# Kernel optimization log

Measured on AMD Instinct MI355X. Metric: run time of the kernel, lower is better.

Reference implementation:

```python
import jax, jax.numpy as jnp
import numpy as np

EPS = 1e-12


def qsplit(x):
    # [..., 4n] with block layout [r|i|j|k] -> [..., n, 4]
    s = x.shape
    n = s[-1] // 4
    return jnp.swapaxes(x.reshape(s[:-1] + (4, n)), -1, -2)


def qmerge(q):
    # [..., n, 4] -> [..., 4n] block layout (transpose(-1,-2).view in torch)
    s = q.shape
    return jnp.swapaxes(q, -1, -2).reshape(s[:-2] + (s[-2] * 4,))


def qnormalize(q):
    # F.normalize(p=2, dim=-1)
    n = jnp.linalg.norm(q, axis=-1, keepdims=True)
    return q / jnp.maximum(n, EPS)


def qmul(q, r):
    # Hamilton product, last axis = (w, x, y, z)
    qw, qx, qy, qz = q[..., 0], q[..., 1], q[..., 2], q[..., 3]
    rw, rx, ry, rz = r[..., 0], r[..., 1], r[..., 2], r[..., 3]
    return jnp.stack([
        qw * rw - qx * rx - qy * ry - qz * rz,
        qw * rx + qx * rw + qy * rz - qz * ry,
        qw * ry - qx * rz + qy * rw + qz * rx,
        qw * rz + qx * ry - qy * rx + qz * rw,
    ], axis=-1)


def qlinear(x, W, b=None):
    # quaternion linear: x [..., 4*n_in], W [4, n_in, n_out]
    xr, xi, xj, xk = jnp.split(x, 4, axis=-1)
    Wr, Wi, Wj, Wk = W[0], W[1], W[2], W[3]
    out = jnp.concatenate([
        xr @ Wr - xi @ Wi - xj @ Wj - xk @ Wk,
        xr @ Wi + xi @ Wr + xj @ Wk - xk @ Wj,
        xr @ Wj - xi @ Wk + xj @ Wr + xk @ Wi,
        xr @ Wk + xi @ Wj - xj @ Wi + xk @ Wr,
    ], axis=-1)
    return out if b is None else out + b


def setup_inputs() -> dict:
    key = jax.random.key(0)
    ks = jax.random.split(key, 7)
    T_enc, T_tgt, B, D, H = 100, 26, 512, 96, 1024
    d4, h4 = D // 4, H // 4
    inp = jax.random.normal(ks[0], (T_enc, B, D), dtype=jnp.float32)
    target = jax.random.normal(ks[1], (T_tgt, B, D), dtype=jnp.float32)
    Wx = jax.random.normal(ks[2], (4, d4, h4), dtype=jnp.float32) * 0.05
    bx = jnp.zeros((H,), dtype=jnp.float32)
    Wh = jax.random.normal(ks[3], (4, h4, h4), dtype=jnp.float32) * 0.05
    Wl = jax.random.normal(ks[4], (4, h4, d4), dtype=jnp.float32) * 0.05
    bl = jnp.zeros((D,), dtype=jnp.float32)
    return {"inp": inp, "target": target, "Wx": Wx, "bx": bx, "Wh": Wh, "Wl": Wl, "bl": bl}


def reference(inp, target, Wx, bx, Wh, Wl, bl):
    B = inp.shape[1]
    H = Wh.shape[1] * 4

    def rnn_step(h, xt):
        h_new = jnp.tanh(qlinear(xt, Wx, bx) + qlinear(h, Wh))
        return h_new, h_new

    def predict(hseq, pre):
        # quaternion linear + per-quaternion L2 normalize + residual Hamilton product
        pred = qlinear(hseq, Wl, bl)
        qn = qnormalize(qsplit(pred))
        return qmerge(qmul(qn, qsplit(pre)))

    h0 = jnp.zeros((B, H), dtype=inp.dtype)
    h_last, hs = jax.lax.scan(rnn_step, h0, inp)  # hs: [T_enc, B, H]
    out_enc = predict(hs, inp)

    def dec_step(carry, _):
        h, x = carry
        h_new = jnp.tanh(qlinear(x, Wx, bx) + qlinear(h, Wh))
        pred = predict(h_new, x)
        return (h_new, pred), pred

    T_dec = target.shape[0] - 1
    _, out_dec = jax.lax.scan(dec_step, (h_last, target[0]), None, length=T_dec)
    return out_enc, out_dec
```

## Files before the change

kernel.cpp:

```cpp
#include <hip/hip_runtime.h>
#include <hip/hip_bf16.h>
#include <cstdint>

#define TENC 100
#define TDEC 25
#define BATCH 512
#define DIN 96
#define HDIM 1024

__device__ __constant__ int q_widx[4][4] = {{0,1,2,3},{1,0,3,2},{2,3,0,1},{3,2,1,0}};
__device__ __constant__ float q_sgn[4][4] = {{1.f,-1.f,-1.f,-1.f},
                                             {1.f, 1.f, 1.f,-1.f},
                                             {1.f,-1.f, 1.f, 1.f},
                                             {1.f, 1.f,-1.f, 1.f}};

__global__ void build_eff_kernel(const float* __restrict__ W, float* __restrict__ M,
                                 int nin, int nout) {
    int idx = blockIdx.x * blockDim.x + threadIdx.x;
    int ncol = nout * 4;
    int total = nin * 4 * ncol;
    if (idx >= total) return;
    int col = idx % ncol;
    int k = idx / ncol;
    int c = k / nin, m = k - c * nin;
    int comp = col / nout, o = col - comp * nout;
    M[idx] = q_sgn[comp][c] * W[(size_t)(q_widx[comp][c] * nin + m) * nout + o];
}

__device__ inline float xla_tanh(float x) {
    float ax = fabsf(x);
    if (ax < 0.0004f) return x;
    float t = fminf(fmaxf(x, -7.99881172180175781f), 7.99881172180175781f);
    float x2 = __fmul_rn(t, t);
    float p = -2.76076847742355e-16f;
    p = __fadd_rn(__fmul_rn(p, x2), 2.00018790482477e-13f);
    p = __fadd_rn(__fmul_rn(p, x2), -8.60467152213735e-11f);
    p = __fadd_rn(__fmul_rn(p, x2), 5.12229709037114e-08f);
    p = __fadd_rn(__fmul_rn(p, x2), 1.48572235717979e-05f);
    p = __fadd_rn(__fmul_rn(p, x2), 6.37261928875436e-04f);
    p = __fadd_rn(__fmul_rn(p, x2), 4.89352455891786e-03f);
    float num = __fmul_rn(t, p);
    float q = 1.19825839466702e-06f;
    q = __fadd_rn(__fmul_rn(q, x2), 1.18534705686654e-04f);
    q = __fadd_rn(__fmul_rn(q, x2), 2.26843463243900e-03f);
    q = __fadd_rn(__fmul_rn(q, x2), 4.89352518554385e-03f);
    return __fdiv_rn(num, q);
}

__global__ __launch_bounds__(256)
void rnn_part(const float* __restrict__ X,
              const float* __restrict__ Hin,
              const float* __restrict__ Mx,
              const float* __restrict__ Mh,
              float* __restrict__ part) {
    __shared__ __align__(16) float As[64][68];
    __shared__ __align__(16) float Bs[64][64];

    const int tid = threadIdx.x;
    const int tx = tid & 15, ty = tid >> 4;
    const int c0 = blockIdx.x * 64;
    const int r0 = blockIdx.y * 64;
    const int z  = blockIdx.z;
    const int lk = tid & 63, lr = tid >> 6;

    float acc[4][4];
    #pragma unroll
    for (int i = 0; i < 4; ++i)
        #pragma unroll
        for (int j = 0; j < 4; ++j) acc[i][j] = 0.f;

    if (z < 4) {
        for (int kb = 0; kb < 4; ++kb) {
            const int k0 = z * 256 + kb * 64;
            __syncthreads();
            {
                const float* ap = Hin + (size_t)(r0 + lr) * 1024 + k0 + lk;
                #pragma unroll
                for (int i = 0; i < 16; ++i)
                    As[lk][lr + 4 * i] = ap[(size_t)(4 * i) * 1024];
            }
            {
                const int ccol = c0 + lk;
                #pragma unroll
                for (int i = 0; i < 16; ++i) {
                    int k = lr + 4 * i;
                    Bs[k][lk] = Mh[(size_t)(k0 + k) * 1024 + ccol];
                }
            }
            __syncthreads();
            #pragma unroll 8
            for (int k = 0; k < 64; ++k) {
                float4 av = *reinterpret_cast<const float4*>(&As[k][ty * 4]);
                float4 bv = *reinterpret_cast<const float4*>(&Bs[k][tx * 4]);
                float aa[4] = {av.x, av.y, av.z, av.w};
                float bb[4] = {bv.x, bv.y, bv.z, bv.w};
                #pragma unroll
                for (int i = 0; i < 4; ++i)
                    #pragma unroll
                    for (int j = 0; j < 4; ++j)
                        acc[i][j] = __fadd_rn(acc[i][j], __fmul_rn(aa[i], bb[j]));
            }
        }
    } else {
        for (int c = 0; c < 4; ++c) {
            float xa[4][4];
            #pragma unroll
            for (int i = 0; i < 4; ++i)
                #pragma unroll
                for (int j = 0; j < 4; ++j) xa[i][j] = 0.f;
            const int k0 = c * 24;
            __syncthreads();
            if (lk < 24) {
                const float* ap = X + (size_t)(r0 + lr) * 96 + k0 + lk;
                #pragma unroll
                for (int i = 0; i < 16; ++i)
                    As[lk][lr + 4 * i] = ap[(size_t)(4 * i) * 96];
            }
            {
                const int ccol = c0 + lk;
                #pragma unroll
                for (int i = 0; i < 16; ++i) {
                    int k = lr + 4 * i;
                    if (k < 24)
                        Bs[k][lk] = Mx[(size_t)(k0 + k) * 1024 + ccol];
                }
            }
            __syncthreads();
            #pragma unroll 4
            for (int k = 0; k < 24; ++k) {
                float4 av = *reinterpret_cast<const float4*>(&As[k][ty * 4]);
                float4 bv = *reinterpret_cast<const float4*>(&Bs[k][tx * 4]);
                float aa[4] = {av.x, av.y, av.z, av.w};
                float bb[4] = {bv.x, bv.y, bv.z, bv.w};
                #pragma unroll
                for (int i = 0; i < 4; ++i)
                    #pragma unroll
                    for (int j = 0; j < 4; ++j)
                        xa[i][j] = __fadd_rn(xa[i][j], __fmul_rn(aa[i], bb[j]));
            }
            #pragma unroll
            for (int i = 0; i < 4; ++i)
                #pragma unroll
                for (int j = 0; j < 4; ++j)
                    acc[i][j] = __fadd_rn(acc[i][j], xa[i][j]);
        }
    }

    float* pp = part + (size_t)z * (BATCH * HDIM);
    const int ccol = c0 + tx * 4;
    #pragma unroll
    for (int i = 0; i < 4; ++i) {
        int r = r0 + ty * 4 + i;
        *reinterpret_cast<float4*>(pp + (size_t)r * 1024 + ccol) =
            make_float4(acc[i][0], acc[i][1], acc[i][2], acc[i][3]);
    }
}

__global__ __launch_bounds__(256)
void rnn_combine(const float* __restrict__ part, const float* __restrict__ bx,
                 float* __restrict__ Hout) {
    int t = blockIdx.x * blockDim.x + threadIdx.x;
    int i = t * 4;
    int col = i & 1023;
    const size_t SH = (size_t)BATCH * HDIM;
    float4 xp = *reinterpret_cast<const float4*>(part + 4 * SH + i);
    float4 h0 = *reinterpret_cast<const float4*>(part + 0 * SH + i);
    float4 h1 = *reinterpret_cast<const float4*>(part + 1 * SH + i);
    float4 h2 = *reinterpret_cast<const float4*>(part + 2 * SH + i);
    float4 h3 = *reinterpret_cast<const float4*>(part + 3 * SH + i);
    float4 bb = *reinterpret_cast<const float4*>(bx + col);
    float o[4];
    {
        float xpv[4] = {xp.x, xp.y, xp.z, xp.w};
        float h0v[4] = {h0.x, h0.y, h0.z, h0.w};
        float h1v[4] = {h1.x, h1.y, h1.z, h1.w};
        float h2v[4] = {h2.x, h2.y, h2.z, h2.w};
        float h3v[4] = {h3.x, h3.y, h3.z, h3.w};
        float bv[4]  = {bb.x, bb.y, bb.z, bb.w};
        #pragma unroll
        for (int j = 0; j < 4; ++j) {
            float hcb = __fadd_rn(__fadd_rn(__fadd_rn(h0v[j], h1v[j]), h2v[j]), h3v[j]);
            float rs  = __fadd_rn(__fadd_rn(xpv[j], bv[j]), hcb);
            o[j] = xla_tanh(rs);
        }
    }
    *reinterpret_cast<float4*>(Hout + i) = make_float4(o[0], o[1], o[2], o[3]);
}

__global__ __launch_bounds__(256)
void predict_part(const float* __restrict__ H,
                  const float* __restrict__ Ml,
                  float* __restrict__ ppart) {
    __shared__ float lds[8576];
    float* As = lds;
    float* Bs = lds + 2176;

    const int tid = threadIdx.x;
    const int tx = tid & 15, ty = tid >> 4;
    const int r0 = blockIdx.x * 32;
    const int z  = blockIdx.y;

    float acc[2][6];
    #pragma unroll
    for (int i = 0; i < 2; ++i)
        #pragma unroll
        for (int j = 0; j < 6; ++j) acc[i][j] = 0.f;

    for (int kb = 0; kb < 4; ++kb) {
        const int k0 = z * 256 + kb * 64;
        __syncthreads();
        {
            int lk = tid & 63, lr0 = tid >> 6;
            #pragma unroll
            for (int i = 0; i < 8; ++i) {
                int row = lr0 + 4 * i;
                As[lk * 34 + row] = H[(size_t)(r0 + row) * 1024 + k0 + lk];
            }
        }
        #pragma unroll
        for (int i = 0; i < 24; ++i) {
            int idx = tid + 256 * i;
            int k = idx / 96, c = idx - k * 96;
            Bs[k * 100 + c] = Ml[(size_t)(k0 + k) * 96 + c];
        }
        __syncthreads();
        #pragma unroll 4
        for (int k = 0; k < 64; ++k) {
            float2 a = *reinterpret_cast<const float2*>(&As[k * 34 + ty * 2]);
            const float* bp = &Bs[k * 100 + tx * 6];
            float2 b0 = *reinterpret_cast<const float2*>(bp);
            float2 b1 = *reinterpret_cast<const float2*>(bp + 2);
            float2 b2 = *reinterpret_cast<const float2*>(bp + 4);
            float bv[6] = {b0.x, b0.y, b1.x, b1.y, b2.x, b2.y};
            #pragma unroll
            for (int j = 0; j < 6; ++j) {
                acc[0][j] = __fadd_rn(acc[0][j], __fmul_rn(a.x, bv[j]));
                acc[1][j] = __fadd_rn(acc[1][j], __fmul_rn(a.y, bv[j]));
            }
        }
    }

    float* pp = ppart + (size_t)z * (BATCH * DIN);
    #pragma unroll
    for (int i = 0; i < 2; ++i)
        #pragma unroll
        for (int j = 0; j < 6; ++j)
            pp[(size_t)(r0 + ty * 2 + i) * 96 + tx * 6 + j] = acc[i][j];
}

__global__ void combine_qmul(const float* __restrict__ ppart,
                             const float* __restrict__ bl,
                             const float* __restrict__ pre,
                             float* __restrict__ out, int M) {
    int q = blockIdx.x * blockDim.x + threadIdx.x;
    if (q >= M * 24) return;
    int b = q / 24, n = q - b * 24;
    const size_t SP = (size_t)BATCH * DIN;
    float pq[4];
    #pragma unroll
    for (int comp = 0; comp < 4; ++comp) {
        size_t idx = (size_t)b * 96 + comp * 24 + n;
        float p0 = ppart[0 * SP + idx];
        float p1 = ppart[1 * SP + idx];
        float p2 = ppart[2 * SP + idx];
        float p3 = ppart[3 * SP + idx];
        pq[comp] = __fadd_rn(__fadd_rn(__fadd_rn(__fadd_rn(p0, p1), p2), p3),
                             bl[comp * 24 + n]);
    }
    float pw = pq[0], px = pq[1], py = pq[2], pz = pq[3];
    float s = __fadd_rn(__fadd_rn(__fadd_rn(__fmul_rn(pw, pw), __fmul_rn(px, px)),
                                  __fmul_rn(py, py)), __fmul_rn(pz, pz));
    float nr = sqrtf(s);
    float nm = fmaxf(nr, 1e-12f);
    pw = __fdiv_rn(pw, nm); px = __fdiv_rn(px, nm);
    py = __fdiv_rn(py, nm); pz = __fdiv_rn(pz, nm);
    const float* r = pre + (size_t)b * 96 + n;
    float rw = r[0], rx = r[24], ry = r[48], rz = r[72];
    float* o = out + (size_t)b * 96 + n;
    o[0]  = __fsub_rn(__fsub_rn(__fsub_rn(__fmul_rn(pw, rw), __fmul_rn(px, rx)),
                                __fmul_rn(py, ry)), __fmul_rn(pz, rz));
    o[24] = __fsub_rn(__fadd_rn(__fadd_rn(__fmul_rn(pw, rx), __fmul_rn(px, rw)),
                                __fmul_rn(py, rz)), __fmul_rn(pz, ry));
    o[48] = __fadd_rn(__fadd_rn(__fsub_rn(__fmul_rn(pw, ry), __fmul_rn(px, rz)),
                                __fmul_rn(py, rw)), __fmul_rn(pz, rx));
    o[72] = __fadd_rn(__fsub_rn(__fadd_rn(__fmul_rn(pw, rz), __fmul_rn(px, ry)),
                                __fmul_rn(py, rx)), __fmul_rn(pz, rw));
}

__global__ __launch_bounds__(256)
void predict_qmul(const float* __restrict__ H,
                  const float* __restrict__ Ml,
                  const float* __restrict__ bl,
                  const float* __restrict__ pre,
                  float* __restrict__ out) {
    __shared__ float lds[8576];
    float* As = lds;
    float* Bs = lds + 2176;
    float* Ps = lds;

    const int tid = threadIdx.x;
    const int tx = tid & 15, ty = tid >> 4;
    const int r0 = blockIdx.x * 32;

    float hcb[2][6], ha[2][6];
    #pragma unroll
    for (int i = 0; i < 2; ++i)
        #pragma unroll
        for (int j = 0; j < 6; ++j) { hcb[i][j] = 0.f; ha[i][j] = 0.f; }

    for (int kb = 0; kb < 16; ++kb) {
        __syncthreads();
        {
            int lk = tid & 63, lr0 = tid >> 6;
            #pragma unroll
            for (int i = 0; i < 8; ++i) {
                int row = lr0 + 4 * i;
                As[lk * 34 + row] = H[(size_t)(r0 + row) * 1024 + kb * 64 + lk];
            }
        }
        #pragma unroll
        for (int i = 0; i < 24; ++i) {
            int idx = tid + 256 * i;
            int k = idx / 96, c = idx - k * 96;
            Bs[k * 100 + c] = Ml[(size_t)(kb * 64 + k) * 96 + c];
        }
        __syncthreads();
        #pragma unroll 4
        for (int k = 0; k < 64; ++k) {
            float2 a = *reinterpret_cast<const float2*>(&As[k * 34 + ty * 2]);
            const float* bp = &Bs[k * 100 + tx * 6];
            float2 b0 = *reinterpret_cast<const float2*>(bp);
            float2 b1 = *reinterpret_cast<const float2*>(bp + 2);
            float2 b2 = *reinterpret_cast<const float2*>(bp + 4);
            float bv[6] = {b0.x, b0.y, b1.x, b1.y, b2.x, b2.y};
            #pragma unroll
            for (int j = 0; j < 6; ++j) {
                ha[0][j] = __fadd_rn(ha[0][j], __fmul_rn(a.x, bv[j]));
                ha[1][j] = __fadd_rn(ha[1][j], __fmul_rn(a.y, bv[j]));
            }
        }
        if ((kb & 3) == 3) {
            #pragma unroll
            for (int i = 0; i < 2; ++i)
                #pragma unroll
                for (int j = 0; j < 6; ++j) {
                    hcb[i][j] = __fadd_rn(hcb[i][j], ha[i][j]);
                    ha[i][j] = 0.f;
                }
        }
    }

    __syncthreads();
    #pragma unroll
    for (int i = 0; i < 2; ++i)
        #pragma unroll
        for (int j = 0; j < 6; ++j) {
            int c = tx * 6 + j;
            Ps[(ty * 2 + i) * 100 + c] = __fadd_rn(hcb[i][j], bl[c]);
        }
    __syncthreads();

    #pragma unroll
    for (int i = 0; i < 3; ++i) {
        int q = tid + 256 * i;
        int row = q / 24, n = q - row * 24;
        const float* p = &Ps[row * 100 + n];
        float pw = p[0], px = p[24], py = p[48], pz = p[72];
        float s = __fadd_rn(__fadd_rn(__fadd_rn(__fmul_rn(pw, pw), __fmul_rn(px, px)),
                                      __fmul_rn(py, py)), __fmul_rn(pz, pz));
        float nr = sqrtf(s);
        float nm = fmaxf(nr, 1e-12f);
        pw = __fdiv_rn(pw, nm); px = __fdiv_rn(px, nm);
        py = __fdiv_rn(py, nm); pz = __fdiv_rn(pz, nm);
        const float* r = pre + (size_t)(r0 + row) * 96 + n;
        float rw = r[0], rx = r[24], ry = r[48], rz = r[72];
        float* o = out + (size_t)(r0 + row) * 96 + n;
        o[0]  = __fsub_rn(__fsub_rn(__fsub_rn(__fmul_rn(pw, rw), __fmul_rn(px, rx)),
                                    __fmul_rn(py, ry)), __fmul_rn(pz, rz));
        o[24] = __fsub_rn(__fadd_rn(__fadd_rn(__fmul_rn(pw, rx), __fmul_rn(px, rw)),
                                    __fmul_rn(py, rz)), __fmul_rn(pz, ry));
        o[48] = __fadd_rn(__fadd_rn(__fsub_rn(__fmul_rn(pw, ry), __fmul_rn(px, rz)),
                                    __fmul_rn(py, rw)), __fmul_rn(pz, rx));
        o[72] = __fadd_rn(__fsub_rn(__fadd_rn(__fmul_rn(pw, rz), __fmul_rn(px, ry)),
                                    __fmul_rn(py, rx)), __fmul_rn(pz, rw));
    }
}

extern "C" void kernel_launch(void* const* d_in, const int* in_sizes, int n_in,
                              void* d_out, int out_size, void* d_ws, size_t ws_size,
                              hipStream_t stream) {
    const float* inp    = (const float*)d_in[0];
    const float* target = (const float*)d_in[1];
    const float* Wx     = (const float*)d_in[2];
    const float* bx     = (const float*)d_in[3];
    const float* Wh     = (const float*)d_in[4];
    const float* Wl     = (const float*)d_in[5];
    const float* bl     = (const float*)d_in[6];

    float* out = (float*)d_out;
    float* out_enc = out;
    float* out_dec = out + (size_t)TENC * BATCH * DIN;

    const size_t SH = (size_t)BATCH * HDIM;
    const size_t SX = (size_t)BATCH * DIN;

    size_t off = 0;
    auto alloc = [&](size_t nf) -> float* {
        float* p = (float*)((char*)d_ws + off);
        off += nf * sizeof(float);
        return p;
    };
    float* M_x   = alloc((size_t)DIN * HDIM);
    float* M_h   = alloc((size_t)HDIM * HDIM);
    float* M_l   = alloc((size_t)HDIM * DIN);
    float* hs    = alloc((size_t)(TENC + 1) * SH);
    float* parts = alloc(5 * SH);
    float* ppart = alloc(4 * SX);

    {
        int t1 = 4 * 24 * 4 * 256;
        build_eff_kernel<<<(t1 + 255) / 256, 256, 0, stream>>>(Wx, M_x, 24, 256);
        int t2 = 4 * 256 * 4 * 256;
        build_eff_kernel<<<(t2 + 255) / 256, 256, 0, stream>>>(Wh, M_h, 256, 256);
        int t3 = 4 * 256 * 4 * 24;
        build_eff_kernel<<<(t3 + 255) / 256, 256, 0, stream>>>(Wl, M_l, 256, 24);
    }

    hipMemsetAsync(hs, 0, SH * sizeof(float), stream);

    dim3 gPart(HDIM / 64, BATCH / 64, 5);
    const int gComb = (int)(SH / 4 / 256);

    for (int t = 0; t < TENC; ++t) {
        rnn_part<<<gPart, 256, 0, stream>>>(
            inp + (size_t)t * SX, hs + (size_t)t * SH, M_x, M_h, parts);
        rnn_combine<<<gComb, 256, 0, stream>>>(parts, bx, hs + (size_t)(t + 1) * SH);
    }
    predict_qmul<<<(TENC * BATCH) / 32, 256, 0, stream>>>(
        hs + SH, M_l, bl, inp, out_enc);

    const float* x = target;
    float* hin = hs + (size_t)TENC * SH;
    dim3 gPPart(BATCH / 32, 4);
    for (int t = 0; t < TDEC; ++t) {
        float* hout = (t & 1) ? (hs + SH) : hs;
        rnn_part<<<gPart, 256, 0, stream>>>(x, hin, M_x, M_h, parts);
        rnn_combine<<<gComb, 256, 0, stream>>>(parts, bx, hout);
        predict_part<<<gPPart, 256, 0, stream>>>(hout, M_l, ppart);
        int nq = BATCH * 24;
        combine_qmul<<<(nq + 255) / 256, 256, 0, stream>>>(
            ppart, bl, x, out_dec + (size_t)t * SX, BATCH);
        x = out_dec + (size_t)t * SX;
        hin = hout;
    }
}
```

Baseline: 4.973 ms.

## Double-buffer RNN GEMM, fold input projection into split blocks, retile predict kernels

```diff
diff --git a/kernel.cpp b/kernel.cpp
--- a/kernel.cpp
+++ b/kernel.cpp
@@ -1,5 +1,4 @@
 #include <hip/hip_runtime.h>
-#include <hip/hip_bf16.h>
 #include <cstdint>
 
 #define TENC 100
@@ -52,9 +51,11 @@
               const float* __restrict__ Hin,
               const float* __restrict__ Mx,
               const float* __restrict__ Mh,
-              float* __restrict__ part) {
-    __shared__ __align__(16) float As[64][68];
-    __shared__ __align__(16) float Bs[64][64];
+              float* __restrict__ parts) {
+    __shared__ __align__(16) float As[2][64][68];
+    __shared__ __align__(16) float Bs[2][64][64];
+    __shared__ __align__(16) float Xs[24][68];
+    __shared__ __align__(16) float Ms[24][64];
 
     const int tid = threadIdx.x;
     const int tx = tid & 15, ty = tid >> 4;
@@ -62,229 +63,143 @@
     const int r0 = blockIdx.y * 64;
     const int z  = blockIdx.z;
     const int lk = tid & 63, lr = tid >> 6;
-
-    float acc[4][4];
-    #pragma unroll
-    for (int i = 0; i < 4; ++i)
-        #pragma unroll
-        for (int j = 0; j < 4; ++j) acc[i][j] = 0.f;
-
-    if (z < 4) {
-        for (int kb = 0; kb < 4; ++kb) {
-            const int k0 = z * 256 + kb * 64;
-            __syncthreads();
-            {
-                const float* ap = Hin + (size_t)(r0 + lr) * 1024 + k0 + lk;
-                #pragma unroll
-                for (int i = 0; i < 16; ++i)
-                    As[lk][lr + 4 * i] = ap[(size_t)(4 * i) * 1024];
-            }
-            {
-                const int ccol = c0 + lk;
-                #pragma unroll
-                for (int i = 0; i < 16; ++i) {
-                    int k = lr + 4 * i;
-                    Bs[k][lk] = Mh[(size_t)(k0 + k) * 1024 + ccol];
-                }
-            }
-            __syncthreads();
-            #pragma unroll 8
-            for (int k = 0; k < 64; ++k) {
-                float4 av = *reinterpret_cast<const float4*>(&As[k][ty * 4]);
-                float4 bv = *reinterpret_cast<const float4*>(&Bs[k][tx * 4]);
-                float aa[4] = {av.x, av.y, av.z, av.w};
-                float bb[4] = {bv.x, bv.y, bv.z, bv.w};
-                #pragma unroll
-                for (int i = 0; i < 4; ++i)
-                    #pragma unroll
-                    for (int j = 0; j < 4; ++j)
-                        acc[i][j] = __fadd_rn(acc[i][j], __fmul_rn(aa[i], bb[j]));
-            }
-        }
-    } else {
-        for (int c = 0; c < 4; ++c) {
-            float xa[4][4];
-            #pragma unroll
-            for (int i = 0; i < 4; ++i)
-                #pragma unroll
-                for (int j = 0; j < 4; ++j) xa[i][j] = 0.f;
-            const int k0 = c * 24;
-            __syncthreads();
-            if (lk < 24) {
-                const float* ap = X + (size_t)(r0 + lr) * 96 + k0 + lk;
-                #pragma unroll
-                for (int i = 0; i < 16; ++i)
-                    As[lk][lr + 4 * i] = ap[(size_t)(4 * i) * 96];
-            }
-            {
-                const int ccol = c0 + lk;
-                #pragma unroll
-                for (int i = 0; i < 16; ++i) {
-                    int k = lr + 4 * i;
-                    if (k < 24)
-                        Bs[k][lk] = Mx[(size_t)(k0 + k) * 1024 + ccol];
-                }
-            }
-            __syncthreads();
-            #pragma unroll 4
-            for (int k = 0; k < 24; ++k) {
-                float4 av = *reinterpret_cast<const float4*>(&As[k][ty * 4]);
-                float4 bv = *reinterpret_cast<const float4*>(&Bs[k][tx * 4]);
-                float aa[4] = {av.x, av.y, av.z, av.w};
-                float bb[4] = {bv.x, bv.y, bv.z, bv.w};
-                #pragma unroll
-                for (int i = 0; i < 4; ++i)
-                    #pragma unroll
-                    for (int j = 0; j < 4; ++j)
-                        xa[i][j] = __fadd_rn(xa[i][j], __fmul_rn(aa[i], bb[j]));
-            }
+    const size_t SH = (size_t)BATCH * HDIM;
+
+    float areg[16], breg[16];
+
+    {
+        const int k0 = z * 256;
+        #pragma unroll
+        for (int i = 0; i < 16; ++i)
+            areg[i] = Hin[(size_t)(r0 + lr + 4 * i) * 1024 + k0 + lk];
+        #pragma unroll
+        for (int i = 0; i < 16; ++i)
+            breg[i] = Mh[(size_t)(k0 + lr + 4 * i) * 1024 + c0 + lk];
+    }
+    #pragma unroll
+    for (int i = 0; i < 6; ++i) {
+        int idx = tid + 256 * i;
+        int row = idx / 24, kk = idx - row * 24;
+        Xs[kk][row] = X[(size_t)(r0 + row) * 96 + z * 24 + kk];
+    }
+    #pragma unroll
+    for (int i = 0; i < 6; ++i) {
+        int idx = tid + 256 * i;
+        int kk = idx >> 6, col = idx & 63;
+        Ms[kk][col] = Mx[(size_t)(z * 24 + kk) * 1024 + c0 + col];
+    }
+    #pragma unroll
+    for (int i = 0; i < 16; ++i) As[0][lk][lr + 4 * i] = areg[i];
+    #pragma unroll
+    for (int i = 0; i < 16; ++i) Bs[0][lr + 4 * i][lk] = breg[i];
+    __syncthreads();
+
+    {
+        float xa[4][4];
+        #pragma unroll
+        for (int i = 0; i < 4; ++i)
+            #pragma unroll
+            for (int j = 0; j < 4; ++j) xa[i][j] = 0.f;
+        #pragma unroll 4
+        for (int kk = 0; kk < 24; ++kk) {
+            float4 av = *reinterpret_cast<const float4*>(&Xs[kk][ty * 4]);
+            float4 bv = *reinterpret_cast<const float4*>(&Ms[kk][tx * 4]);
+            float aa[4] = {av.x, av.y, av.z, av.w};
+            float bb[4] = {bv.x, bv.y, bv.z, bv.w};
             #pragma unroll
             for (int i = 0; i < 4; ++i)
                 #pragma unroll
                 for (int j = 0; j < 4; ++j)
-                    acc[i][j] = __fadd_rn(acc[i][j], xa[i][j]);
-        }
-    }
-
-    float* pp = part + (size_t)z * (BATCH * HDIM);
+                    xa[i][j] = __fadd_rn(xa[i][j], __fmul_rn(aa[i], bb[j]));
+        }
+        float* pp = parts + (size_t)(4 + z) * SH;
+        const int ccol = c0 + tx * 4;
+        #pragma unroll
+        for (int i = 0; i < 4; ++i)
+            *reinterpret_cast<float4*>(pp + (size_t)(r0 + ty * 4 + i) * 1024 + ccol) =
+                make_float4(xa[i][0], xa[i][1], xa[i][2], xa[i][3]);
+    }
+
+    float acc[4][4];
+    #pragma unroll
+    for (int i = 0; i < 4; ++i)
+        #pragma unroll
+        for (int j = 0; j < 4; ++j) acc[i][j] = 0.f;
+
+    for (int kb = 0; kb < 4; ++kb) {
+        const int cur = kb & 1;
+        if (kb < 3) {
+            const int k0 = z * 256 + (kb + 1) * 64;
+            #pragma unroll
+            for (int i = 0; i < 16; ++i)
+                areg[i] = Hin[(size_t)(r0 + lr + 4 * i) * 1024 + k0 + lk];
+            #pragma unroll
+            for (int i = 0; i < 16; ++i)
+                breg[i] = Mh[(size_t)(k0 + lr + 4 * i) * 1024 + c0 + lk];
+        }
+        #pragma unroll 8
+        for (int k = 0; k < 64; ++k) {
+            float4 av = *reinterpret_cast<const float4*>(&As[cur][k][ty * 4]);
+            float4 bv = *reinterpret_cast<const float4*>(&Bs[cur][k][tx * 4]);
+            float aa[4] = {av.x, av.y, av.z, av.w};
+            float bb[4] = {bv.x, bv.y, bv.z, bv.w};
+            #pragma unroll
+            for (int i = 0; i < 4; ++i)
+                #pragma unroll
+                for (int j = 0; j < 4; ++j)
+                    acc[i][j] = __fadd_rn(acc[i][j], __fmul_rn(aa[i], bb[j]));
+        }
+        if (kb < 3) {
+            #pragma unroll
+            for (int i = 0; i < 16; ++i) As[cur ^ 1][lk][lr + 4 * i] = areg[i];
+            #pragma unroll
+            for (int i = 0; i < 16; ++i) Bs[cur ^ 1][lr + 4 * i][lk] = breg[i];
+            __syncthreads();
+        }
+    }
+
+    float* pp = parts + (size_t)z * SH;
     const int ccol = c0 + tx * 4;
     #pragma unroll
-    for (int i = 0; i < 4; ++i) {
-        int r = r0 + ty * 4 + i;
-        *reinterpret_cast<float4*>(pp + (size_t)r * 1024 + ccol) =
+    for (int i = 0; i < 4; ++i)
+        *reinterpret_cast<float4*>(pp + (size_t)(r0 + ty * 4 + i) * 1024 + ccol) =
             make_float4(acc[i][0], acc[i][1], acc[i][2], acc[i][3]);
-    }
 }
 
 __global__ __launch_bounds__(256)
-void rnn_combine(const float* __restrict__ part, const float* __restrict__ bx,
+void rnn_combine(const float* __restrict__ parts, const float* __restrict__ bx,
                  float* __restrict__ Hout) {
     int t = blockIdx.x * blockDim.x + threadIdx.x;
     int i = t * 4;
     int col = i & 1023;
     const size_t SH = (size_t)BATCH * HDIM;
-    float4 xp = *reinterpret_cast<const float4*>(part + 4 * SH + i);
-    float4 h0 = *reinterpret_cast<const float4*>(part + 0 * SH + i);
-    float4 h1 = *reinterpret_cast<const float4*>(part + 1 * SH + i);
-    float4 h2 = *reinterpret_cast<const float4*>(part + 2 * SH + i);
-    float4 h3 = *reinterpret_cast<const float4*>(part + 3 * SH + i);
+    float4 h0 = *reinterpret_cast<const float4*>(parts + 0 * SH + i);
+    float4 h1 = *reinterpret_cast<const float4*>(parts + 1 * SH + i);
+    float4 h2 = *reinterpret_cast<const float4*>(parts + 2 * SH + i);
+    float4 h3 = *reinterpret_cast<const float4*>(parts + 3 * SH + i);
+    float4 x0 = *reinterpret_cast<const float4*>(parts + 4 * SH + i);
+    float4 x1 = *reinterpret_cast<const float4*>(parts + 5 * SH + i);
+    float4 x2 = *reinterpret_cast<const float4*>(parts + 6 * SH + i);
+    float4 x3 = *reinterpret_cast<const float4*>(parts + 7 * SH + i);
     float4 bb = *reinterpret_cast<const float4*>(bx + col);
+    float h0v[4] = {h0.x, h0.y, h0.z, h0.w};
+    float h1v[4] = {h1.x, h1.y, h1.z, h1.w};
+    float h2v[4] = {h2.x, h2.y, h2.z, h2.w};
+    float h3v[4] = {h3.x, h3.y, h3.z, h3.w};
+    float x0v[4] = {x0.x, x0.y, x0.z, x0.w};
+    float x1v[4] = {x1.x, x1.y, x1.z, x1.w};
+    float x2v[4] = {x2.x, x2.y, x2.z, x2.w};
+    float x3v[4] = {x3.x, x3.y, x3.z, x3.w};
+    float bv[4]  = {bb.x, bb.y, bb.z, bb.w};
     float o[4];
-    {
-        float xpv[4] = {xp.x, xp.y, xp.z, xp.w};
-        float h0v[4] = {h0.x, h0.y, h0.z, h0.w};
-        float h1v[4] = {h1.x, h1.y, h1.z, h1.w};
-        float h2v[4] = {h2.x, h2.y, h2.z, h2.w};
-        float h3v[4] = {h3.x, h3.y, h3.z, h3.w};
-        float bv[4]  = {bb.x, bb.y, bb.z, bb.w};
-        #pragma unroll
-        for (int j = 0; j < 4; ++j) {
-            float hcb = __fadd_rn(__fadd_rn(__fadd_rn(h0v[j], h1v[j]), h2v[j]), h3v[j]);
-            float rs  = __fadd_rn(__fadd_rn(xpv[j], bv[j]), hcb);
-            o[j] = xla_tanh(rs);
-        }
+    #pragma unroll
+    for (int j = 0; j < 4; ++j) {
+        float xcb = __fadd_rn(__fadd_rn(__fadd_rn(x0v[j], x1v[j]), x2v[j]), x3v[j]);
+        float hcb = __fadd_rn(__fadd_rn(__fadd_rn(h0v[j], h1v[j]), h2v[j]), h3v[j]);
+        float rs  = __fadd_rn(__fadd_rn(xcb, bv[j]), hcb);
+        o[j] = xla_tanh(rs);
     }
     *reinterpret_cast<float4*>(Hout + i) = make_float4(o[0], o[1], o[2], o[3]);
-}
-
-__global__ __launch_bounds__(256)
-void predict_part(const float* __restrict__ H,
-                  const float* __restrict__ Ml,
-                  float* __restrict__ ppart) {
-    __shared__ float lds[8576];
-    float* As = lds;
-    float* Bs = lds + 2176;
-
-    const int tid = threadIdx.x;
-    const int tx = tid & 15, ty = tid >> 4;
-    const int r0 = blockIdx.x * 32;
-    const int z  = blockIdx.y;
-
-    float acc[2][6];
-    #pragma unroll
-    for (int i = 0; i < 2; ++i)
-        #pragma unroll
-        for (int j = 0; j < 6; ++j) acc[i][j] = 0.f;
-
-    for (int kb = 0; kb < 4; ++kb) {
-        const int k0 = z * 256 + kb * 64;
-        __syncthreads();
-        {
-            int lk = tid & 63, lr0 = tid >> 6;
-            #pragma unroll
-            for (int i = 0; i < 8; ++i) {
-                int row = lr0 + 4 * i;
-                As[lk * 34 + row] = H[(size_t)(r0 + row) * 1024 + k0 + lk];
-            }
-        }
-        #pragma unroll
-        for (int i = 0; i < 24; ++i) {
-            int idx = tid + 256 * i;
-            int k = idx / 96, c = idx - k * 96;
-            Bs[k * 100 + c] = Ml[(size_t)(k0 + k) * 96 + c];
-        }
-        __syncthreads();
-        #pragma unroll 4
-        for (int k = 0; k < 64; ++k) {
-            float2 a = *reinterpret_cast<const float2*>(&As[k * 34 + ty * 2]);
-            const float* bp = &Bs[k * 100 + tx * 6];
-            float2 b0 = *reinterpret_cast<const float2*>(bp);
-            float2 b1 = *reinterpret_cast<const float2*>(bp + 2);
-            float2 b2 = *reinterpret_cast<const float2*>(bp + 4);
-            float bv[6] = {b0.x, b0.y, b1.x, b1.y, b2.x, b2.y};
-            #pragma unroll
-            for (int j = 0; j < 6; ++j) {
-                acc[0][j] = __fadd_rn(acc[0][j], __fmul_rn(a.x, bv[j]));
-                acc[1][j] = __fadd_rn(acc[1][j], __fmul_rn(a.y, bv[j]));
-            }
-        }
-    }
-
-    float* pp = ppart + (size_t)z * (BATCH * DIN);
-    #pragma unroll
-    for (int i = 0; i < 2; ++i)
-        #pragma unroll
-        for (int j = 0; j < 6; ++j)
-            pp[(size_t)(r0 + ty * 2 + i) * 96 + tx * 6 + j] = acc[i][j];
-}
-
-__global__ void combine_qmul(const float* __restrict__ ppart,
-                             const float* __restrict__ bl,
-                             const float* __restrict__ pre,
-                             float* __restrict__ out, int M) {
-    int q = blockIdx.x * blockDim.x + threadIdx.x;
-    if (q >= M * 24) return;
-    int b = q / 24, n = q - b * 24;
-    const size_t SP = (size_t)BATCH * DIN;
-    float pq[4];
-    #pragma unroll
-    for (int comp = 0; comp < 4; ++comp) {
-        size_t idx = (size_t)b * 96 + comp * 24 + n;
-        float p0 = ppart[0 * SP + idx];
-        float p1 = ppart[1 * SP + idx];
-        float p2 = ppart[2 * SP + idx];
-        float p3 = ppart[3 * SP + idx];
-        pq[comp] = __fadd_rn(__fadd_rn(__fadd_rn(__fadd_rn(p0, p1), p2), p3),
-                             bl[comp * 24 + n]);
-    }
-    float pw = pq[0], px = pq[1], py = pq[2], pz = pq[3];
-    float s = __fadd_rn(__fadd_rn(__fadd_rn(__fmul_rn(pw, pw), __fmul_rn(px, px)),
-                                  __fmul_rn(py, py)), __fmul_rn(pz, pz));
-    float nr = sqrtf(s);
-    float nm = fmaxf(nr, 1e-12f);
-    pw = __fdiv_rn(pw, nm); px = __fdiv_rn(px, nm);
-    py = __fdiv_rn(py, nm); pz = __fdiv_rn(pz, nm);
-    const float* r = pre + (size_t)b * 96 + n;
-    float rw = r[0], rx = r[24], ry = r[48], rz = r[72];
-    float* o = out + (size_t)b * 96 + n;
-    o[0]  = __fsub_rn(__fsub_rn(__fsub_rn(__fmul_rn(pw, rw), __fmul_rn(px, rx)),
-                                __fmul_rn(py, ry)), __fmul_rn(pz, rz));
-    o[24] = __fsub_rn(__fadd_rn(__fadd_rn(__fmul_rn(pw, rx), __fmul_rn(px, rw)),
-                                __fmul_rn(py, rz)), __fmul_rn(pz, ry));
-    o[48] = __fadd_rn(__fadd_rn(__fsub_rn(__fmul_rn(pw, ry), __fmul_rn(px, rz)),
-                                __fmul_rn(py, rw)), __fmul_rn(pz, rx));
-    o[72] = __fadd_rn(__fsub_rn(__fadd_rn(__fmul_rn(pw, rz), __fmul_rn(px, ry)),
-                                __fmul_rn(py, rx)), __fmul_rn(pz, rw));
 }
 
 __global__ __launch_bounds__(256)
@@ -293,31 +208,27 @@
                   const float* __restrict__ bl,
                   const float* __restrict__ pre,
                   float* __restrict__ out) {
-    __shared__ float lds[8576];
+    __shared__ float lds[10752];
     float* As = lds;
-    float* Bs = lds + 2176;
+    float* Bs = lds + 4352;
     float* Ps = lds;
 
     const int tid = threadIdx.x;
     const int tx = tid & 15, ty = tid >> 4;
-    const int r0 = blockIdx.x * 32;
-
-    float hcb[2][6], ha[2][6];
-    #pragma unroll
-    for (int i = 0; i < 2; ++i)
+    const int r0 = blockIdx.x * 64;
+    const int lk = tid & 63, lr = tid >> 6;
+
+    float hcb[4][6], ha[4][6];
+    #pragma unroll
+    for (int i = 0; i < 4; ++i)
         #pragma unroll
         for (int j = 0; j < 6; ++j) { hcb[i][j] = 0.f; ha[i][j] = 0.f; }
 
     for (int kb = 0; kb < 16; ++kb) {
         __syncthreads();
-        {
-            int lk = tid & 63, lr0 = tid >> 6;
-            #pragma unroll
-            for (int i = 0; i < 8; ++i) {
-                int row = lr0 + 4 * i;
-                As[lk * 34 + row] = H[(size_t)(r0 + row) * 1024 + kb * 64 + lk];
-            }
-        }
+        #pragma unroll
+        for (int i = 0; i < 16; ++i)
+            As[lk * 68 + lr + 4 * i] = H[(size_t)(r0 + lr + 4 * i) * 1024 + kb * 64 + lk];
         #pragma unroll
         for (int i = 0; i < 24; ++i) {
             int idx = tid + 256 * i;
@@ -327,21 +238,22 @@
         __syncthreads();
         #pragma unroll 4
         for (int k = 0; k < 64; ++k) {
-            float2 a = *reinterpret_cast<const float2*>(&As[k * 34 + ty * 2]);
+            float4 av = *reinterpret_cast<const float4*>(&As[k * 68 + ty * 4]);
             const float* bp = &Bs[k * 100 + tx * 6];
             float2 b0 = *reinterpret_cast<const float2*>(bp);
             float2 b1 = *reinterpret_cast<const float2*>(bp + 2);
             float2 b2 = *reinterpret_cast<const float2*>(bp + 4);
-            float bv[6] = {b0.x, b0.y, b1.x, b1.y, b2.x, b2.y};
-            #pragma unroll
-            for (int j = 0; j < 6; ++j) {
-                ha[0][j] = __fadd_rn(ha[0][j], __fmul_rn(a.x, bv[j]));
-                ha[1][j] = __fadd_rn(ha[1][j], __fmul_rn(a.y, bv[j]));
-            }
+            float aa[4] = {av.x, av.y, av.z, av.w};
+            float bb[6] = {b0.x, b0.y, b1.x, b1.y, b2.x, b2.y};
+            #pragma unroll
+            for (int i = 0; i < 4; ++i)
+                #pragma unroll
+                for (int j = 0; j < 6; ++j)
+                    ha[i][j] = __fadd_rn(ha[i][j], __fmul_rn(aa[i], bb[j]));
         }
         if ((kb & 3) == 3) {
             #pragma unroll
-            for (int i = 0; i < 2; ++i)
+            for (int i = 0; i < 4; ++i)
                 #pragma unroll
                 for (int j = 0; j < 6; ++j) {
                     hcb[i][j] = __fadd_rn(hcb[i][j], ha[i][j]);
@@ -352,16 +264,16 @@
 
     __syncthreads();
     #pragma unroll
-    for (int i = 0; i < 2; ++i)
+    for (int i = 0; i < 4; ++i)
         #pragma unroll
         for (int j = 0; j < 6; ++j) {
             int c = tx * 6 + j;
-            Ps[(ty * 2 + i) * 100 + c] = __fadd_rn(hcb[i][j], bl[c]);
+            Ps[(ty * 4 + i) * 100 + c] = __fadd_rn(hcb[i][j], bl[c]);
         }
     __syncthreads();
 
     #pragma unroll
-    for (int i = 0; i < 3; ++i) {
+    for (int i = 0; i < 6; ++i) {
         int q = tid + 256 * i;
         int row = q / 24, n = q - row * 24;
         const float* p = &Ps[row * 100 + n];
@@ -386,6 +298,97 @@
     }
 }
 
+__global__ __launch_bounds__(256)
+void predict_part(const float* __restrict__ H,
+                  const float* __restrict__ Ml,
+                  float* __restrict__ ppart) {
+    __shared__ float As[64][18];
+    __shared__ float Bs[64][100];
+
+    const int tid = threadIdx.x;
+    const int tx = tid & 15, ty = tid >> 4;
+    const int r0 = blockIdx.x * 16;
+    const int z  = blockIdx.y;
+
+    float acc[6];
+    #pragma unroll
+    for (int j = 0; j < 6; ++j) acc[j] = 0.f;
+
+    for (int kb = 0; kb < 4; ++kb) {
+        const int k0 = z * 256 + kb * 64;
+        __syncthreads();
+        #pragma unroll
+        for (int i = 0; i < 4; ++i) {
+            int idx = tid + 256 * i;
+            int k = idx & 63, row = idx >> 6;
+            As[k][row] = H[(size_t)(r0 + row) * 1024 + k0 + k];
+        }
+        #pragma unroll
+        for (int i = 0; i < 24; ++i) {
+            int idx = tid + 256 * i;
+            int k = idx / 96, c = idx - k * 96;
+            Bs[k][c] = Ml[(size_t)(k0 + k) * 96 + c];
+        }
+        __syncthreads();
+        #pragma unroll 8
+        for (int k = 0; k < 64; ++k) {
+            float a = As[k][ty];
+            const float* bp = &Bs[k][tx * 6];
+            float2 b0 = *reinterpret_cast<const float2*>(bp);
+            float2 b1 = *reinterpret_cast<const float2*>(bp + 2);
+            float2 b2 = *reinterpret_cast<const float2*>(bp + 4);
+            float bb[6] = {b0.x, b0.y, b1.x, b1.y, b2.x, b2.y};
+            #pragma unroll
+            for (int j = 0; j < 6; ++j)
+                acc[j] = __fadd_rn(acc[j], __fmul_rn(a, bb[j]));
+        }
+    }
+
+    float* pp = ppart + (size_t)z * (BATCH * DIN);
+    #pragma unroll
+    for (int j = 0; j < 6; ++j)
+        pp[(size_t)(r0 + ty) * 96 + tx * 6 + j] = acc[j];
+}
+
+__global__ void combine_qmul(const float* __restrict__ ppart,
+                             const float* __restrict__ bl,
+                             const float* __restrict__ pre,
+                             float* __restrict__ out, int M) {
+    int q = blockIdx.x * blockDim.x + threadIdx.x;
+    if (q >= M * 24) return;
+    int b = q / 24, n = q - b * 24;
+    const size_t SP = (size_t)BATCH * DIN;
+    float pq[4];
+    #pragma unroll
+    for (int comp = 0; comp < 4; ++comp) {
+        size_t idx = (size_t)b * 96 + comp * 24 + n;
+        float p0 = ppart[0 * SP + idx];
+        float p1 = ppart[1 * SP + idx];
+        float p2 = ppart[2 * SP + idx];
+        float p3 = ppart[3 * SP + idx];
+        pq[comp] = __fadd_rn(__fadd_rn(__fadd_rn(__fadd_rn(p0, p1), p2), p3),
+                             bl[comp * 24 + n]);
+    }
+    float pw = pq[0], px = pq[1], py = pq[2], pz = pq[3];
+    float s = __fadd_rn(__fadd_rn(__fadd_rn(__fmul_rn(pw, pw), __fmul_rn(px, px)),
+                                  __fmul_rn(py, py)), __fmul_rn(pz, pz));
+    float nr = sqrtf(s);
+    float nm = fmaxf(nr, 1e-12f);
+    pw = __fdiv_rn(pw, nm); px = __fdiv_rn(px, nm);
+    py = __fdiv_rn(py, nm); pz = __fdiv_rn(pz, nm);
+    const float* r = pre + (size_t)b * 96 + n;
+    float rw = r[0], rx = r[24], ry = r[48], rz = r[72];
+    float* o = out + (size_t)b * 96 + n;
+    o[0]  = __fsub_rn(__fsub_rn(__fsub_rn(__fmul_rn(pw, rw), __fmul_rn(px, rx)),
+                                __fmul_rn(py, ry)), __fmul_rn(pz, rz));
+    o[24] = __fsub_rn(__fadd_rn(__fadd_rn(__fmul_rn(pw, rx), __fmul_rn(px, rw)),
+                                __fmul_rn(py, rz)), __fmul_rn(pz, ry));
+    o[48] = __fadd_rn(__fadd_rn(__fsub_rn(__fmul_rn(pw, ry), __fmul_rn(px, rz)),
+                                __fmul_rn(py, rw)), __fmul_rn(pz, rx));
+    o[72] = __fadd_rn(__fsub_rn(__fadd_rn(__fmul_rn(pw, rz), __fmul_rn(px, ry)),
+                                __fmul_rn(py, rx)), __fmul_rn(pz, rw));
+}
+
 extern "C" void kernel_launch(void* const* d_in, const int* in_sizes, int n_in,
                               void* d_out, int out_size, void* d_ws, size_t ws_size,
                               hipStream_t stream) {
@@ -414,7 +417,7 @@
     float* M_h   = alloc((size_t)HDIM * HDIM);
     float* M_l   = alloc((size_t)HDIM * DIN);
     float* hs    = alloc((size_t)(TENC + 1) * SH);
-    float* parts = alloc(5 * SH);
+    float* parts = alloc(8 * SH);
     float* ppart = alloc(4 * SX);
 
     {
@@ -428,7 +431,7 @@
 
     hipMemsetAsync(hs, 0, SH * sizeof(float), stream);
 
-    dim3 gPart(HDIM / 64, BATCH / 64, 5);
+    dim3 gPart(HDIM / 64, BATCH / 64, 4);
     const int gComb = (int)(SH / 4 / 256);
 
     for (int t = 0; t < TENC; ++t) {
@@ -436,12 +439,12 @@
             inp + (size_t)t * SX, hs + (size_t)t * SH, M_x, M_h, parts);
         rnn_combine<<<gComb, 256, 0, stream>>>(parts, bx, hs + (size_t)(t + 1) * SH);
     }
-    predict_qmul<<<(TENC * BATCH) / 32, 256, 0, stream>>>(
+    predict_qmul<<<(TENC * BATCH) / 64, 256, 0, stream>>>(
         hs + SH, M_l, bl, inp, out_enc);
 
     const float* x = target;
     float* hin = hs + (size_t)TENC * SH;
-    dim3 gPPart(BATCH / 32, 4);
+    dim3 gPPart(BATCH / 16, 4);
     for (int t = 0; t < TDEC; ++t) {
         float* hout = (t & 1) ? (hs + SH) : hs;
         rnn_part<<<gPart, 256, 0, stream>>>(x, hin, M_x, M_h, parts);
```

New measurement: 3.980 ms, median of 2. 1.25x faster.
